# Kernel optimization log

Hardware: AMD Instinct MI355X
Metric: run time of the kernel (lower is better)

## Reference

```python
import jax, jax.numpy as jnp
import numpy as np

N = 100000  # num nodes
E = 1600000  # num edges
D_IN = 64
D_OUT = 64


def setup_inputs() -> dict:
    key = jax.random.key(0)
    k = jax.random.split(key, 8)
    x = jax.random.normal(k[0], (N, D_IN), dtype=jnp.float32)
    edge_index = jax.random.randint(k[1], (2, E), 0, N, dtype=jnp.int64)
    s1 = 1.0 / np.sqrt(D_IN)
    s2 = 1.0 / np.sqrt(D_OUT)
    W1 = jax.random.uniform(k[2], (D_IN, D_OUT), jnp.float32, -s1, s1)
    b1 = jax.random.uniform(k[3], (D_OUT,), jnp.float32, -s1, s1)
    W2 = jax.random.uniform(k[4], (D_OUT, D_OUT), jnp.float32, -s2, s2)
    b2 = jax.random.uniform(k[5], (D_OUT,), jnp.float32, -s2, s2)
    eps = jnp.asarray(0.0, dtype=jnp.float32)  # learnable (train_eps=True)
    return {"x": x, "edge_index": edge_index, "W1": W1, "b1": b1, "W2": W2, "b2": b2, "eps": eps}


def reference(x, edge_index, W1, b1, W2, b2, eps):
    src, dst = edge_index[0], edge_index[1]
    # sum-aggregate neighbor features: agg[i] = sum_{(j->i)} x[j]
    agg = jax.ops.segment_sum(x[src], dst, num_segments=N)  # [N, D_IN]
    h = (1.0 + eps) * x + agg
    h = jax.nn.relu(h @ W1 + b1)
    return h @ W2 + b2
```

## Files before the change

kernel.cpp:

```cpp
#include <hip/hip_runtime.h>

#define NN 100000
#define NE 1600000
#define D  64
#define NPB 196
#define NBK 512
#define RPL 8
#define CAPR 512
#define CHUNK 2048
#define EPT (CHUNK / 256)
#define NCH ((NE + CHUNK - 1) / CHUNK)
#define CVTB ((NN * D / 16 + 255) / 256)
#define WSTR 72


typedef unsigned short u16;
typedef __attribute__((ext_vector_type(8))) short bf16x8;
typedef __attribute__((ext_vector_type(4))) float f32x4;

__device__ __forceinline__ u16 f32_to_bf16_rn(float f) {
    unsigned u = __float_as_uint(f);
    return (u16)((u + 0x7FFF + ((u >> 16) & 1)) >> 16);
}
__device__ __forceinline__ unsigned pk2(float lo, float hi) {
    return (unsigned)f32_to_bf16_rn(lo) | ((unsigned)f32_to_bf16_rn(hi) << 16);
}
__device__ __forceinline__ float bf16_to_f32(u16 h) {
    return __uint_as_float(((unsigned)h) << 16);
}

__global__ __launch_bounds__(256) void bin_cvt_kernel(const float* __restrict__ x,
                                                      u16* __restrict__ xb,
                                                      const int* __restrict__ ei,
                                                      int* __restrict__ cursor,
                                                      int* __restrict__ bins) {
    __shared__ int lc[NBK];
    __shared__ int lbase[NBK];
    const int t = threadIdx.x;

    if (blockIdx.x >= NCH) {
        int i = ((blockIdx.x - NCH) * 256 + t) * 16;
        if (i < NN * D) {
            float4 a = *(const float4*)(x + i);
            float4 b = *(const float4*)(x + i + 4);
            float4 c = *(const float4*)(x + i + 8);
            float4 d = *(const float4*)(x + i + 12);
            uint4 o1, o2;
            o1.x = pk2(a.x, a.y); o1.y = pk2(a.z, a.w);
            o1.z = pk2(b.x, b.y); o1.w = pk2(b.z, b.w);
            o2.x = pk2(c.x, c.y); o2.y = pk2(c.z, c.w);
            o2.z = pk2(d.x, d.y); o2.w = pk2(d.z, d.w);
            *(uint4*)(xb + i) = o1;
            *(uint4*)(xb + i + 8) = o2;
        }
        return;
    }

    const int base = blockIdx.x * CHUNK;
    const int rep  = blockIdx.x & (RPL - 1);

    int dsts[EPT];
    #pragma unroll
    for (int j = 0; j < EPT; ++j) {
        int e = base + t + j * 256;
        dsts[j] = (e < NE) ? ei[NE + e] : -1;
    }

    for (int i = t; i < NBK; i += 256) lc[i] = 0;
    __syncthreads();
    #pragma unroll
    for (int j = 0; j < EPT; ++j)
        if (dsts[j] >= 0) atomicAdd(&lc[(unsigned)dsts[j] / NPB], 1);
    __syncthreads();
    for (int i = t; i < NBK; i += 256) {
        int c = lc[i];
        lbase[i] = c ? atomicAdd(&cursor[rep * NBK + i], c) : 0;
        lc[i] = 0;
    }
    __syncthreads();
    #pragma unroll
    for (int j = 0; j < EPT; ++j) {
        if (dsts[j] >= 0) {
            int src = ei[base + t + j * 256];
            int dst = dsts[j];
            int b   = (unsigned)dst / NPB;
            int loc = dst - b * NPB;
            int o   = atomicAdd(&lc[b], 1);
            int pos = lbase[b] + o;
            if (pos < CAPR)
                bins[(b * RPL + rep) * CAPR + pos] = (loc << 17) | src;
        }
    }
}

__global__ __launch_bounds__(1024) void agg_kernel(const float* __restrict__ x,
                                                   const u16* __restrict__ xb,
                                                   const float* __restrict__ eps,
                                                   const int* __restrict__ cursor,
                                                   const int* __restrict__ bins,
                                                   u16* __restrict__ hb) {
    __shared__ int sorted[RPL * CAPR];
    __shared__ int tmp[256];
    __shared__ int off[256];
    __shared__ int cur[256];
    const int b    = blockIdx.x;
    const int t    = threadIdx.x;
    const int lane = t & 63;
    const int w    = t >> 6;
    const float e1 = 1.0f + *eps;

    if (t < 256) tmp[t] = 0;
    __syncthreads();
    int nrep[RPL];
    #pragma unroll
    for (int r = 0; r < RPL; ++r) nrep[r] = min(cursor[r * NBK + b], CAPR);
    #pragma unroll
    for (int r = 0; r < RPL; ++r) {
        const int rb = (b * RPL + r) * CAPR;
        for (int i = t; i < nrep[r]; i += 1024)
            atomicAdd(&tmp[bins[rb + i] >> 17], 1);
    }
    __syncthreads();
    int v = (t < 256) ? tmp[t] : 0;
    for (int o = 1; o < 256; o <<= 1) {
        int u = (t < 256 && t >= o) ? tmp[t - o] : 0;
        __syncthreads();
        if (t < 256) tmp[t] += u;
        __syncthreads();
    }
    if (t < 256) { off[t] = tmp[t] - v; cur[t] = tmp[t] - v; }
    __syncthreads();
    #pragma unroll
    for (int r = 0; r < RPL; ++r) {
        const int rb = (b * RPL + r) * CAPR;
        for (int i = t; i < nrep[r]; i += 1024) {
            int pk  = bins[rb + i];
            int pos = atomicAdd(&cur[pk >> 17], 1);
            sorted[pos] = pk & 0x1FFFF;
        }
    }
    __syncthreads();

    #pragma unroll
    for (int j = 0; j < 13; ++j) {
        int r = w + 16 * j;
        if (r < NPB) {
            int node = b * NPB + r;
            if (node < NN) {
                float a = e1 * x[node * D + lane];
                int p  = off[r];
                int pe = off[r + 1];
                for (; p + 8 <= pe; p += 8) {
                    int i0 = sorted[p],     i1 = sorted[p + 1];
                    int i2 = sorted[p + 2], i3 = sorted[p + 3];
                    int i4 = sorted[p + 4], i5 = sorted[p + 5];
                    int i6 = sorted[p + 6], i7 = sorted[p + 7];
                    float v0 = bf16_to_f32(xb[i0 * D + lane]);
                    float v1 = bf16_to_f32(xb[i1 * D + lane]);
                    float v2 = bf16_to_f32(xb[i2 * D + lane]);
                    float v3 = bf16_to_f32(xb[i3 * D + lane]);
                    float v4 = bf16_to_f32(xb[i4 * D + lane]);
                    float v5 = bf16_to_f32(xb[i5 * D + lane]);
                    float v6 = bf16_to_f32(xb[i6 * D + lane]);
                    float v7 = bf16_to_f32(xb[i7 * D + lane]);
                    a += ((v0 + v1) + (v2 + v3)) + ((v4 + v5) + (v6 + v7));
                }
                for (; p + 4 <= pe; p += 4) {
                    int i0 = sorted[p],     i1 = sorted[p + 1];
                    int i2 = sorted[p + 2], i3 = sorted[p + 3];
                    float v0 = bf16_to_f32(xb[i0 * D + lane]);
                    float v1 = bf16_to_f32(xb[i1 * D + lane]);
                    float v2 = bf16_to_f32(xb[i2 * D + lane]);
                    float v3 = bf16_to_f32(xb[i3 * D + lane]);
                    a += (v0 + v1) + (v2 + v3);
                }
                for (; p < pe; ++p) a += bf16_to_f32(xb[sorted[p] * D + lane]);
                hb[node * D + lane] = f32_to_bf16_rn(a);
            }
        }
    }
}

__global__ __launch_bounds__(256, 2) void mlp_mfma_kernel(
        const u16* __restrict__ hb, float* __restrict__ out,
        const float* __restrict__ W1, const float* __restrict__ b1,
        const float* __restrict__ W2, const float* __restrict__ b2) {
    __shared__ u16 wt1[D * WSTR];
    __shared__ u16 wt2[D * WSTR];
    __shared__ u16 lds[4][16 * WSTR];
    const int lane = threadIdx.x & 63;
    const int wv   = threadIdx.x >> 6;
    const int m    = lane & 15;
    const int q    = lane >> 4;
    u16* tile = &lds[wv][0];

    for (int i = threadIdx.x; i < D * D; i += 256) {
        int k = i >> 6, n = i & 63;
        wt1[n * WSTR + k] = f32_to_bf16_rn(W1[i]);
        wt2[n * WSTR + k] = f32_to_bf16_rn(W2[i]);
    }
    __syncthreads();

    bf16x8 wb1[4][2], wb2[4][2];
    #pragma unroll
    for (int t = 0; t < 4; ++t)
        #pragma unroll
        for (int s = 0; s < 2; ++s) {
            const int o = (t * 16 + m) * WSTR + s * 32 + q * 8;
            wb1[t][s] = *(const bf16x8*)&wt1[o];
            wb2[t][s] = *(const bf16x8*)&wt2[o];
        }
    float bias1[4], bias2[4];
    #pragma unroll
    for (int t = 0; t < 4; ++t) {
        bias1[t] = b1[t * 16 + m];
        bias2[t] = b2[t * 16 + m];
    }

    const int wave = blockIdx.x * 4 + wv;
    const int nw   = gridDim.x * 4;
    for (int ti = wave; ti < NN / 16; ti += nw) {
        const int rowbase = ti * 16;

        bf16x8 a1f[2];
        #pragma unroll
        for (int s = 0; s < 2; ++s)
            a1f[s] = *(const bf16x8*)(hb + (rowbase + m) * D + s * 32 + q * 8);

        #pragma unroll
        for (int t = 0; t < 4; ++t) {
            f32x4 cc = {0.f, 0.f, 0.f, 0.f};
            cc = __builtin_amdgcn_mfma_f32_16x16x32_bf16(a1f[0], wb1[t][0], cc, 0, 0, 0);
            cc = __builtin_amdgcn_mfma_f32_16x16x32_bf16(a1f[1], wb1[t][1], cc, 0, 0, 0);
            #pragma unroll
            for (int r = 0; r < 4; ++r) {
                float vv = fmaxf(cc[r] + bias1[t], 0.0f);
                tile[(q * 4 + r) * WSTR + t * 16 + m] = f32_to_bf16_rn(vv);
            }
        }

        bf16x8 a2f[2];
        #pragma unroll
        for (int s = 0; s < 2; ++s)
            a2f[s] = *(const bf16x8*)&tile[m * WSTR + s * 32 + q * 8];

        #pragma unroll
        for (int t = 0; t < 4; ++t) {
            f32x4 cc = {0.f, 0.f, 0.f, 0.f};
            cc = __builtin_amdgcn_mfma_f32_16x16x32_bf16(a2f[0], wb2[t][0], cc, 0, 0, 0);
            cc = __builtin_amdgcn_mfma_f32_16x16x32_bf16(a2f[1], wb2[t][1], cc, 0, 0, 0);
            #pragma unroll
            for (int r = 0; r < 4; ++r)
                out[(rowbase + q * 4 + r) * D + t * 16 + m] = cc[r] + bias2[t];
        }
    }
}

extern "C" void kernel_launch(void* const* d_in, const int* in_sizes, int n_in,
                              void* d_out, int out_size, void* d_ws, size_t ws_size,
                              hipStream_t stream) {
    const float* x   = (const float*)d_in[0];
    const int*   ei  = (const int*)d_in[1];
    const float* W1  = (const float*)d_in[2];
    const float* b1  = (const float*)d_in[3];
    const float* W2  = (const float*)d_in[4];
    const float* b2  = (const float*)d_in[5];
    const float* eps = (const float*)d_in[6];
    float*       out = (float*)d_out;

    int* cursor = (int*)d_ws;
    int* bins   = cursor + RPL * NBK;
    u16* xb     = (u16*)(bins + NBK * RPL * CAPR);
    u16* hb     = xb + NN * D;

    hipMemsetAsync(cursor, 0, RPL * NBK * sizeof(int), stream);
    bin_cvt_kernel<<<NCH + CVTB, 256, 0, stream>>>(x, xb, ei, cursor, bins);
    agg_kernel<<<NBK, 1024, 0, stream>>>(x, xb, eps, cursor, bins, hb);
    mlp_mfma_kernel<<<512, 256, 0, stream>>>(hb, out, W1, b1, W2, b2);
}
```

Before: 153.6 us.

## Pad global bin cursors, rotate atomic order, and register-cache bin entries

Each global bin cursor is padded to its own 64-byte slot, and every binning block starts its cursor reservations at a rotated offset. Both changes aim to cut contention on the global atomics. Source indices are now loaded together with destinations at the start, instead of in the scatter loop. The aggregation kernel reads each replica's bin entries into registers once and reuses them for the histogram and the scatter, replacing two strided passes over global memory. In exchange, the cursor memset and workspace footprint grow 16x, and the register caching depends on CAPR not exceeding the block size.

```diff
diff --git a/kernel.cpp b/kernel.cpp
--- a/kernel.cpp
+++ b/kernel.cpp
@@ -6,6 +6,7 @@
 #define NPB 196
 #define NBK 512
 #define RPL 8
+#define CS  16
 #define CAPR 512
 #define CHUNK 2048
 #define EPT (CHUNK / 256)
@@ -58,12 +59,14 @@
 
     const int base = blockIdx.x * CHUNK;
     const int rep  = blockIdx.x & (RPL - 1);
-
-    int dsts[EPT];
+    const int rot  = ((blockIdx.x >> 3) & 31) << 4;
+
+    int dsts[EPT], srcs[EPT];
     #pragma unroll
     for (int j = 0; j < EPT; ++j) {
         int e = base + t + j * 256;
         dsts[j] = (e < NE) ? ei[NE + e] : -1;
+        srcs[j] = (e < NE) ? ei[e] : 0;
     }
 
     for (int i = t; i < NBK; i += 256) lc[i] = 0;
@@ -72,23 +75,23 @@
     for (int j = 0; j < EPT; ++j)
         if (dsts[j] >= 0) atomicAdd(&lc[(unsigned)dsts[j] / NPB], 1);
     __syncthreads();
-    for (int i = t; i < NBK; i += 256) {
+    for (int ii = t; ii < NBK; ii += 256) {
+        int i = (ii + rot) & (NBK - 1);
         int c = lc[i];
-        lbase[i] = c ? atomicAdd(&cursor[rep * NBK + i], c) : 0;
+        lbase[i] = c ? atomicAdd(&cursor[(rep * NBK + i) * CS], c) : 0;
         lc[i] = 0;
     }
     __syncthreads();
     #pragma unroll
     for (int j = 0; j < EPT; ++j) {
         if (dsts[j] >= 0) {
-            int src = ei[base + t + j * 256];
             int dst = dsts[j];
             int b   = (unsigned)dst / NPB;
             int loc = dst - b * NPB;
             int o   = atomicAdd(&lc[b], 1);
             int pos = lbase[b] + o;
             if (pos < CAPR)
-                bins[(b * RPL + rep) * CAPR + pos] = (loc << 17) | src;
+                bins[(b * RPL + rep) * CAPR + pos] = (loc << 17) | srcs[j];
         }
     }
 }
@@ -110,16 +113,16 @@
     const float e1 = 1.0f + *eps;
 
     if (t < 256) tmp[t] = 0;
-    __syncthreads();
-    int nrep[RPL];
-    #pragma unroll
-    for (int r = 0; r < RPL; ++r) nrep[r] = min(cursor[r * NBK + b], CAPR);
+    int vals[RPL];
     #pragma unroll
     for (int r = 0; r < RPL; ++r) {
-        const int rb = (b * RPL + r) * CAPR;
-        for (int i = t; i < nrep[r]; i += 1024)
-            atomicAdd(&tmp[bins[rb + i] >> 17], 1);
-    }
+        int n = min(cursor[(r * NBK + b) * CS], CAPR);
+        vals[r] = (t < n) ? bins[(b * RPL + r) * CAPR + t] : -1;
+    }
+    __syncthreads();
+    #pragma unroll
+    for (int r = 0; r < RPL; ++r)
+        if (vals[r] >= 0) atomicAdd(&tmp[vals[r] >> 17], 1);
     __syncthreads();
     int v = (t < 256) ? tmp[t] : 0;
     for (int o = 1; o < 256; o <<= 1) {
@@ -132,11 +135,9 @@
     __syncthreads();
     #pragma unroll
     for (int r = 0; r < RPL; ++r) {
-        const int rb = (b * RPL + r) * CAPR;
-        for (int i = t; i < nrep[r]; i += 1024) {
-            int pk  = bins[rb + i];
-            int pos = atomicAdd(&cur[pk >> 17], 1);
-            sorted[pos] = pk & 0x1FFFF;
+        if (vals[r] >= 0) {
+            int pos = atomicAdd(&cur[vals[r] >> 17], 1);
+            sorted[pos] = vals[r] & 0x1FFFF;
         }
     }
     __syncthreads();
@@ -269,11 +270,11 @@
     float*       out = (float*)d_out;
 
     int* cursor = (int*)d_ws;
-    int* bins   = cursor + RPL * NBK;
+    int* bins   = cursor + RPL * NBK * CS;
     u16* xb     = (u16*)(bins + NBK * RPL * CAPR);
     u16* hb     = xb + NN * D;
 
-    hipMemsetAsync(cursor, 0, RPL * NBK * sizeof(int), stream);
+    hipMemsetAsync(cursor, 0, RPL * NBK * CS * sizeof(int), stream);
     bin_cvt_kernel<<<NCH + CVTB, 256, 0, stream>>>(x, xb, ei, cursor, bins);
     agg_kernel<<<NBK, 1024, 0, stream>>>(x, xb, eps, cursor, bins, hb);
     mlp_mfma_kernel<<<512, 256, 0, stream>>>(hb, out, W1, b1, W2, b2);
```

Measured after the change: 160.9 us. 1.05x slower.
